# Optimization experiments

Hardware: AMD Instinct MI355X
Metric: run time of the kernel (lower is better)

## Reference

```python
import jax, jax.numpy as jnp
import numpy as np

N_USERS = 120000
N_ITEMS = 80000
N_NODES = N_USERS + N_ITEMS
D = 64
H = 2
DK = 32
DV = 32
N_LAYERS = 3
N_EDGES = 1280000
B = 4096
TEMPERATURE = 1.0


def setup_inputs() -> dict:
    key = jax.random.key(0)
    ks = jax.random.split(key, 11)
    glorot = lambda k, shape: jax.random.normal(k, shape, dtype=jnp.float32) * np.sqrt(2.0 / (shape[0] + int(np.prod(shape[1:]))))
    return {
        "edge_src": jax.random.randint(ks[0], (N_EDGES,), 0, N_NODES, dtype=jnp.int32),
        "edge_dst": jax.random.randint(ks[1], (N_EDGES,), 0, N_NODES, dtype=jnp.int32),
        # normalized adjacency values (positive, small) like D^-1/2 A D^-1/2 entries
        "edge_val": jax.random.uniform(ks[2], (N_EDGES,), dtype=jnp.float32) * 0.2,
        "U_emb": jax.random.normal(ks[3], (N_USERS, D), dtype=jnp.float32) * 0.01,
        "V_emb": jax.random.normal(ks[4], (N_ITEMS, D), dtype=jnp.float32) * 0.01,
        "Wq": glorot(ks[5], (D, H, DK)),
        "Wk": glorot(ks[6], (D, H, DK)),
        "Wv": glorot(ks[7], (D, H, DV)),
        "Wo": glorot(ks[8], (H * DV, D)),
        "u": jax.random.randint(ks[9], (B,), 0, N_USERS, dtype=jnp.int32),
        "i": jax.random.randint(ks[10], (B,), 0, N_ITEMS, dtype=jnp.int32),
    }


def reference(edge_src, edge_dst, edge_val, U_emb, V_emb, Wq, Wk, Wv, Wo, u, i):
    E0 = jnp.concatenate([U_emb, V_emb], axis=0)  # (N, d)

    # LightGCN propagation: E_{l+1} = A_norm @ E_l via edge-list scatter-add
    def prop(E, _):
        msg = edge_val[:, None] * E[edge_src]                      # (E, d) gather
        En = jax.ops.segment_sum(msg, edge_dst, num_segments=N_NODES)  # (N, d) scatter
        return En, En

    _, layer_outs = jax.lax.scan(prop, E0, None, length=N_LAYERS)
    Es = jnp.concatenate([E0[None], layer_outs], axis=0)  # (L, N, d), L = n_layers+1

    # Layer-wise QKV attention: Q from E0, K/V from every layer
    Q = jnp.einsum('nd,dhk->nhk', E0, Wq)        # (N, H, dk)
    K = jnp.einsum('lnd,dhk->lnhk', Es, Wk)      # (L, N, H, dk)
    V = jnp.einsum('lnd,dhv->lnhv', Es, Wv)      # (L, N, H, dv)
    scale = jnp.sqrt(jnp.asarray(DK, dtype=Q.dtype))
    scores = jnp.einsum('lnhk,nhk->lnh', K, Q) / scale
    alphas = jax.nn.softmax(scores / TEMPERATURE, axis=0)  # softmax over layers
    heads = jnp.einsum('lnh,lnhv->nhv', alphas, V)          # (N, H, dv)
    E_out = heads.reshape(N_NODES, H * DV) @ Wo             # (N, d)

    # score(u, i): dot product of final user/item embeddings
    Ue = E_out[u]
    Ie = E_out[N_USERS + i]
    return jnp.sum(Ue * Ie, axis=1)  # (B,)
```

## Files before the change

### kernel.cpp

```cpp
#include <hip/hip_runtime.h>
#include <hip/hip_fp16.h>

#define NU 120000
#define NI 80000
#define NN 200000
#define DD 64
#define NE 1280000
#define BB 4096
#define NS 8192
#define NB2 196
#define BCAP 8192
#define CH2 2048
#define CB 625

#define FB 196
#define CONVB 3125
#define PREPB 64
#define BSB 32
#define P1B 2048
#define G0B 512
#define NLB 32

__global__ void k_pre(int* __restrict__ bcur, int* __restrict__ n2cnt) {
  int t = threadIdx.x;
  if (t < NB2) bcur[t] = 0;
  if (t == 0) *n2cnt = 0;
}

__global__ void k_coarse2(const int* __restrict__ src, const int* __restrict__ dst,
                          const float* __restrict__ val, int* __restrict__ bcur,
                          int2* __restrict__ c_sv) {
  __shared__ int2 sv[CH2];
  __shared__ unsigned char map8[CH2];
  __shared__ int hist[256];
  __shared__ int lbase[256];
  __shared__ int gbase[256];
  __shared__ int s[256];
  int t = threadIdx.x;
  hist[t] = 0;
  __syncthreads();
  int e0 = blockIdx.x * CH2;
  int d_[CH2 / 256];
#pragma unroll
  for (int k = 0; k < CH2 / 256; ++k) {
    int e = e0 + k * 256 + t;
    d_[k] = (e < NE) ? dst[e] : -1;
    if (d_[k] >= 0) atomicAdd(&hist[d_[k] >> 10], 1);
  }
  __syncthreads();
  int x = hist[t];
  s[t] = x;
  __syncthreads();
  for (int off = 1; off < 256; off <<= 1) {
    int v = (t >= off) ? s[t - off] : 0;
    __syncthreads();
    s[t] += v;
    __syncthreads();
  }
  int lb = s[t] - x;
  lbase[t] = lb;
  gbase[t] = (x && t < NB2) ? (t * BCAP + atomicAdd(&bcur[t], x)) : 0;
  for (int k = lb; k < lb + x; ++k) map8[k] = (unsigned char)t;
  hist[t] = 0;
  __syncthreads();
#pragma unroll
  for (int k = 0; k < CH2 / 256; ++k) {
    int e = e0 + k * 256 + t;
    if (d_[k] >= 0) {
      int b = d_[k] >> 10;
      int lp = lbase[b] + atomicAdd(&hist[b], 1);
      sv[lp] = make_int2(src[e] | ((d_[k] & 1023) << 18), __float_as_int(val[e]));
    }
  }
  __syncthreads();
  int nval = NE - e0;
  if (nval > CH2) nval = CH2;
  for (int sidx = t; sidx < nval; sidx += 256) {
    int b = map8[sidx];
    c_sv[(size_t)gbase[b] + sidx - lbase[b]] = sv[sidx];
  }
}

__device__ __forceinline__ void d_conv(int rel, const float4* __restrict__ U4,
                                       const float4* __restrict__ V4, uint2* __restrict__ H0) {
  int t = threadIdx.x;
  float4 r[4];
#pragma unroll
  for (int k = 0; k < 4; ++k) {
    int idx = rel * 1024 + k * 256 + t;
    int node = idx >> 4, q = idx & 15;
    r[k] = (node < NU) ? U4[(size_t)node * 16 + q] : V4[(size_t)(node - NU) * 16 + q];
  }
#pragma unroll
  for (int k = 0; k < 4; ++k) {
    int idx = rel * 1024 + k * 256 + t;
    __half2 a = __floats2half2_rn(r[k].x, r[k].y);
    __half2 b = __floats2half2_rn(r[k].z, r[k].w);
    uint2 o;
    o.x = __builtin_bit_cast(unsigned int, a);
    o.y = __builtin_bit_cast(unsigned int, b);
    H0[idx] = o;
  }
}

__device__ __forceinline__ void d_prep(int rel, const float* __restrict__ Wq,
                                       const float* __restrict__ Wk, const float* __restrict__ Wv,
                                       const float* __restrict__ Wo, float* __restrict__ Mt,
                                       float* __restrict__ P) {
  int t = rel * 256 + threadIdx.x;
  if (t < 8192) {
    int h = t >> 12;
    int b = (t >> 6) & 63;
    int j = t & 63;
    float s = 0.f;
    for (int k = 0; k < 32; ++k) s += Wk[j * 64 + h * 32 + k] * Wq[b * 64 + h * 32 + k];
    Mt[h * 4096 + b * 64 + j] = s;
  } else if (t < 16384) {
    int t2 = t - 8192;
    int h = t2 >> 12;
    int d = (t2 >> 6) & 63;
    int j = t2 & 63;
    float s = 0.f;
    for (int v = 0; v < 32; ++v) s += Wv[d * 64 + h * 32 + v] * Wo[(h * 32 + v) * 64 + j];
    P[h * 4096 + d * 64 + j] = s;
  }
}

__global__ void k_fine4m(const int* __restrict__ bcur, const int2* __restrict__ c_sv,
                         int2* __restrict__ pairs, int* __restrict__ row_ptr,
                         const float4* __restrict__ U4, const float4* __restrict__ V4,
                         uint2* __restrict__ H0, const float* __restrict__ Wq,
                         const float* __restrict__ Wk, const float* __restrict__ Wv,
                         const float* __restrict__ Wo, float* __restrict__ Mt,
                         float* __restrict__ P, const int* __restrict__ u,
                         const int* __restrict__ ii, int* __restrict__ snodes) {
  __shared__ int cnt[1024];
  __shared__ int pre[1024];
  __shared__ int cur[1024];
  __shared__ int s[256];
  __shared__ int bs[256];
  int b = blockIdx.x, t = threadIdx.x;
  if (b >= FB) {
    int r = b - FB;
    if (r < CONVB) {
      d_conv(r, U4, V4, H0);
    } else if (r < CONVB + PREPB) {
      d_prep(r - CONVB, Wq, Wk, Wv, Wo, Mt, P);
    } else {
      int tt = (r - CONVB - PREPB) * 256 + t;
      if (tt < NS) snodes[tt] = (tt < BB) ? u[tt] : NU + ii[tt - BB];
    }
    return;
  }
  int bc = (t < NB2) ? bcur[t] : 0;
  bs[t] = bc;
  __syncthreads();
  for (int off = 1; off < 256; off <<= 1) {
    int v = (t >= off) ? bs[t - off] : 0;
    __syncthreads();
    bs[t] += v;
    __syncthreads();
  }
  int segN = bcur[b];
  int out0 = bs[b] - segN;
  int seg0 = b * BCAP;
  for (int k = t; k < 1024; k += 256) cnt[k] = 0;
  __syncthreads();
  for (int e = t; e < segN; e += 256) atomicAdd(&cnt[(c_sv[seg0 + e].x >> 18) & 1023], 1);
  __syncthreads();
  int a0 = cnt[4 * t], a1 = cnt[4 * t + 1], a2 = cnt[4 * t + 2], a3 = cnt[4 * t + 3];
  int tot = a0 + a1 + a2 + a3;
  s[t] = tot;
  __syncthreads();
  for (int off = 1; off < 256; off <<= 1) {
    int v = (t >= off) ? s[t - off] : 0;
    __syncthreads();
    s[t] += v;
    __syncthreads();
  }
  int base = s[t] - tot;
  pre[4 * t] = base;
  pre[4 * t + 1] = base + a0;
  pre[4 * t + 2] = base + a0 + a1;
  pre[4 * t + 3] = base + a0 + a1 + a2;
  int node0 = b << 10;
#pragma unroll
  for (int k = 0; k < 4; ++k) {
    int n = node0 + 4 * t + k;
    if (n < NN) row_ptr[n] = out0 + pre[4 * t + k];
  }
  if (b == 0 && t == 0) row_ptr[NN] = NE;
  for (int k = t; k < 1024; k += 256) cur[k] = 0;
  __syncthreads();
  for (int e = t; e < segN; e += 256) {
    int2 svv = c_sv[seg0 + e];
    int ld = (svv.x >> 18) & 1023;
    int off = atomicAdd(&cur[ld], 1);
    pairs[out0 + pre[ld] + off] = make_int2(svv.x & 0x3FFFF, svv.y);
  }
}

template <int ULIST, int BYPOS, int OUTF32>
__device__ __forceinline__ void d_prop8(const uint4* __restrict__ Hin4,
                                        uint4* __restrict__ Hout4, float4* __restrict__ Fout,
                                        const int* __restrict__ row_ptr,
                                        const int2* __restrict__ pairs,
                                        const int* __restrict__ list,
                                        const int* __restrict__ countp, int cconst, int relbid,
                                        int nblk) {
  int n = countp ? *countp : cconst;
  int lane = threadIdx.x & 63;
  int c = lane & 7;
  int gb = lane & 56;
  int gstride = (nblk * 256) >> 3;
  for (int gid = (relbid * 256 + (int)threadIdx.x) >> 3; gid < n; gid += gstride) {
    int node = ULIST ? list[gid] : gid;
    int start = row_ptr[node], end = row_ptr[node + 1];
    float4 a0 = make_float4(0.f, 0.f, 0.f, 0.f);
    float4 a1 = make_float4(0.f, 0.f, 0.f, 0.f);
    for (int t0 = start; t0 < end; t0 += 8) {
      int cap = end - t0;
      if (cap > 8) cap = 8;
      int2 mp = pairs[t0 + (c < cap ? c : 0)];
      uint4 r[8];
      float vv[8];
#pragma unroll
      for (int k = 0; k < 8; ++k) {
        int srclane = gb + k;
        int sidx = __shfl(mp.x, srclane);
        float v = __int_as_float(__shfl(mp.y, srclane));
        vv[k] = (k < cap) ? v : 0.f;
        r[k] = Hin4[(size_t)sidx * 8 + c];
      }
#pragma unroll
      for (int k = 0; k < 8; ++k) {
        float2 f0 = __half22float2(__builtin_bit_cast(__half2, r[k].x));
        float2 f1 = __half22float2(__builtin_bit_cast(__half2, r[k].y));
        float2 f2 = __half22float2(__builtin_bit_cast(__half2, r[k].z));
        float2 f3 = __half22float2(__builtin_bit_cast(__half2, r[k].w));
        a0.x += vv[k] * f0.x;
        a0.y += vv[k] * f0.y;
        a0.z += vv[k] * f1.x;
        a0.w += vv[k] * f1.y;
        a1.x += vv[k] * f2.x;
        a1.y += vv[k] * f2.y;
        a1.z += vv[k] * f3.x;
        a1.w += vv[k] * f3.y;
      }
    }
    size_t op = BYPOS ? (size_t)gid : (size_t)node;
    if (OUTF32) {
      Fout[op * 16 + 2 * c] = a0;
      Fout[op * 16 + 2 * c + 1] = a1;
    } else {
      uint4 o;
      o.x = __builtin_bit_cast(unsigned int, __floats2half2_rn(a0.x, a0.y));
      o.y = __builtin_bit_cast(unsigned int, __floats2half2_rn(a0.z, a0.w));
      o.z = __builtin_bit_cast(unsigned int, __floats2half2_rn(a1.x, a1.y));
      o.w = __builtin_bit_cast(unsigned int, __floats2half2_rn(a1.z, a1.w));
      Hout4[op * 8 + c] = o;
    }
  }
}

__device__ __forceinline__ void d_gather_h(int rel, const uint2* __restrict__ Htab,
                                           float4* __restrict__ Es_l,
                                           const int* __restrict__ snodes) {
  int t = rel * 256 + threadIdx.x;
  if (t >= NS * 16) return;
  int p = t >> 4, q = t & 15;
  int node = snodes[p];
  uint2 r = Htab[(size_t)node * 16 + q];
  float2 f0 = __half22float2(__builtin_bit_cast(__half2, r.x));
  float2 f1 = __half22float2(__builtin_bit_cast(__half2, r.y));
  Es_l[p * 16 + q] = make_float4(f0.x, f0.y, f1.x, f1.y);
}

__global__ void k_prop1m(const uint4* __restrict__ H04, uint4* __restrict__ H14,
                         const float4* __restrict__ U4, const float4* __restrict__ V4,
                         float4* __restrict__ Es0, const int* __restrict__ snodes,
                         const int* __restrict__ row_ptr, const int2* __restrict__ pairs,
                         int* __restrict__ n2list, int* __restrict__ n2cnt) {
  int b = blockIdx.x;
  if (b < P1B) {
    d_prop8<0, 0, 0>(H04, H14, nullptr, row_ptr, pairs, nullptr, nullptr, NN, b, P1B);
  } else if (b < P1B + G0B) {
    int t = (b - P1B) * 256 + threadIdx.x;
    if (t < NS * 16) {
      int p = t >> 4, q = t & 15;
      int node = snodes[p];
      Es0[p * 16 + q] =
          (node < NU) ? U4[(size_t)node * 16 + q] : V4[(size_t)(node - NU) * 16 + q];
    }
  } else {
    int idx = (b - P1B - G0B) * 256 + threadIdx.x;
    if (idx < NS) {
      int node = snodes[idx];
      int s0 = row_ptr[node], e0 = row_ptr[node + 1];
      int pos = atomicAdd(n2cnt, e0 - s0 + 1);
      n2list[pos++] = node;
      for (int j = s0; j < e0; ++j) n2list[pos++] = pairs[j].x;
    }
  }
}

__global__ void k_stage2(const uint4* __restrict__ H14, uint4* __restrict__ H24,
                         const uint2* __restrict__ H1, float4* __restrict__ Es1,
                         const int* __restrict__ snodes, const int* __restrict__ row_ptr,
                         const int2* __restrict__ pairs, const int* __restrict__ n2list,
                         const int* __restrict__ n2cnt) {
  int b = blockIdx.x;
  if (b < 512) {
    d_gather_h(b, H1, Es1, snodes);
  } else {
    d_prop8<1, 0, 0>(H14, H24, nullptr, row_ptr, pairs, n2list, n2cnt, 0, b - 512, 1024);
  }
}

__global__ void k_stage3(const uint4* __restrict__ H24, const uint2* __restrict__ H2,
                         float4* __restrict__ Es2, float4* __restrict__ Es3,
                         const int* __restrict__ snodes, const int* __restrict__ row_ptr,
                         const int2* __restrict__ pairs) {
  int b = blockIdx.x;
  if (b < 512) {
    d_gather_h(b, H2, Es2, snodes);
  } else {
    d_prop8<1, 1, 1>(H24, nullptr, Es3, row_ptr, pairs, snodes, nullptr, NS, b - 512, 512);
  }
}

__global__ void k_attn3(const float* __restrict__ Es, const float* __restrict__ Mt,
                        const float* __restrict__ P, float* __restrict__ out) {
  __shared__ float sb[4][3 * 64];
  int wv = threadIdx.x >> 6, lane = threadIdx.x & 63;
  int w = blockIdx.x * 4 + wv;
  if (w >= BB) return;
  const float inv_scale = 0.17677669529663687f;
  const float* M0 = Mt;
  const float* M1 = Mt + 4096;
  const float* P0 = P;
  const float* P1 = P + 4096;
  float eo[2];
#pragma unroll
  for (int side = 0; side < 2; ++side) {
    int p = side ? (BB + w) : w;
    float e0 = Es[(size_t)0 * NS * DD + p * DD + lane];
    float e1 = Es[(size_t)1 * NS * DD + p * DD + lane];
    float e2 = Es[(size_t)2 * NS * DD + p * DD + lane];
    float e3 = Es[(size_t)3 * NS * DD + p * DD + lane];
    sb[wv][lane] = e0;

    float g0 = 0.f, g1 = 0.f;
#pragma unroll 8
    for (int b = 0; b < 64; ++b) {
      float eb = sb[wv][b];
      g0 = fmaf(M0[b * 64 + lane], eb, g0);
      g1 = fmaf(M1[b * 64 + lane], eb, g1);
    }

    float el[4] = {e0, e1, e2, e3};
    float sc[4][2];
#pragma unroll
    for (int l = 0; l < 4; ++l) {
      float p0 = el[l] * g0, p1 = el[l] * g1;
#pragma unroll
      for (int o = 32; o; o >>= 1) {
        p0 += __shfl_xor(p0, o);
        p1 += __shfl_xor(p1, o);
      }
      sc[l][0] = p0 * inv_scale;
      sc[l][1] = p1 * inv_scale;
    }

    float ebar[2];
#pragma unroll
    for (int h = 0; h < 2; ++h) {
      float m = fmaxf(fmaxf(sc[0][h], sc[1][h]), fmaxf(sc[2][h], sc[3][h]));
      float x0 = expf(sc[0][h] - m), x1 = expf(sc[1][h] - m);
      float x2 = expf(sc[2][h] - m), x3 = expf(sc[3][h] - m);
      float inv = 1.f / (x0 + x1 + x2 + x3);
      ebar[h] = (x0 * e0 + x1 * e1 + x2 * e2 + x3 * e3) * inv;
    }
    sb[wv][64 + lane] = ebar[0];
    sb[wv][128 + lane] = ebar[1];

    float o = 0.f;
#pragma unroll 8
    for (int d = 0; d < 64; ++d) {
      float b0 = sb[wv][64 + d];
      float b1 = sb[wv][128 + d];
      o = fmaf(P0[d * 64 + lane], b0, o);
      o = fmaf(P1[d * 64 + lane], b1, o);
    }
    eo[side] = o;
  }
  float pd = eo[0] * eo[1];
#pragma unroll
  for (int o = 32; o; o >>= 1) pd += __shfl_xor(pd, o);
  if (lane == 0) out[w] = pd;
}

extern "C" void kernel_launch(void* const* d_in, const int* in_sizes, int n_in,
                              void* d_out, int out_size, void* d_ws, size_t ws_size,
                              hipStream_t stream) {
  const int* edge_src = (const int*)d_in[0];
  const int* edge_dst = (const int*)d_in[1];
  const float* edge_val = (const float*)d_in[2];
  const float* U_emb = (const float*)d_in[3];
  const float* V_emb = (const float*)d_in[4];
  const float* Wq = (const float*)d_in[5];
  const float* Wk = (const float*)d_in[6];
  const float* Wv = (const float*)d_in[7];
  const float* Wo = (const float*)d_in[8];
  const int* u = (const int*)d_in[9];
  const int* ii = (const int*)d_in[10];
  float* out = (float*)d_out;

  const float4* U4 = (const float4*)U_emb;
  const float4* V4 = (const float4*)V_emb;

  float* Ea = (float*)d_ws;
  float* Eb = Ea + (size_t)NN * DD;
  float* Es = Eb + (size_t)NN * DD;
  float* Mt = Es + (size_t)4 * NS * DD;
  float* Pm = Mt + 8192;
  int* row_ptr = (int*)(Pm + 8192);
  int* bcur = row_ptr + NN + 4;
  int* snodes = bcur + NB2;
  int* n2cnt = snodes + NS;
  uintptr_t pa = (uintptr_t)(n2cnt + 1);
  pa = (pa + 15) & ~(uintptr_t)15;
  int2* pairs = (int2*)pa;

  uint2* H0 = (uint2*)Ea;
  uint2* H1 = H0 + (size_t)NN * 16;
  uint2* H2 = (uint2*)Eb;
  int2* c_sv = (int2*)Eb;
  int* n2list = (int*)(Es + (size_t)3 * NS * DD);

  float4* Es4 = (float4*)Es;

  k_pre<<<1, 256, 0, stream>>>(bcur, n2cnt);
  k_coarse2<<<CB, 256, 0, stream>>>(edge_src, edge_dst, edge_val, bcur, c_sv);
  k_fine4m<<<FB + CONVB + PREPB + BSB, 256, 0, stream>>>(bcur, c_sv, pairs, row_ptr, U4, V4, H0,
                                                         Wq, Wk, Wv, Wo, Mt, Pm, u, ii, snodes);
  k_prop1m<<<P1B + G0B + NLB, 256, 0, stream>>>((const uint4*)H0, (uint4*)H1, U4, V4,
                                                Es4 + (size_t)0 * NS * 16, snodes, row_ptr, pairs,
                                                n2list, n2cnt);
  k_stage2<<<512 + 1024, 256, 0, stream>>>((const uint4*)H1, (uint4*)H2, H1,
                                           Es4 + (size_t)1 * NS * 16, snodes, row_ptr, pairs,
                                           n2list, n2cnt);
  k_stage3<<<512 + 512, 256, 0, stream>>>((const uint4*)H2, H2, Es4 + (size_t)2 * NS * 16,
                                          Es4 + (size_t)3 * NS * 16, snodes, row_ptr, pairs);
  k_attn3<<<(BB + 3) / 4, 256, 0, stream>>>(Es, Mt, Pm, out);
}
```

Before: 134.7 us.

## Merge pipeline stages into one persistent cooperative kernel with grid syncs

Replaces the seven kernel launches with one cooperative persistent kernel of 512 blocks that runs the phases with grid-stride loops separated by grid.sync(). It also rebalances the work: the coarse bucketing chunk size changes and the prep, zeroing and conversion work is merged into one phase. This removes launch gaps and the tail effects between stages. In exchange each phase gets fewer blocks, so the memory-bound propagation stages may have less parallelism, and every grid barrier has a cost. A fallback multi-kernel path runs if the cooperative launch fails.

```diff
diff --git a/kernel.cpp b/kernel.cpp
--- a/kernel.cpp
+++ b/kernel.cpp
@@ -1,5 +1,6 @@
 #include <hip/hip_runtime.h>
 #include <hip/hip_fp16.h>
+#include <hip/hip_cooperative_groups.h>
 
 #define NU 120000
 #define NI 80000
@@ -10,194 +11,209 @@
 #define NS 8192
 #define NB2 196
 #define BCAP 8192
-#define CH2 2048
-#define CB 625
-
-#define FB 196
-#define CONVB 3125
-#define PREPB 64
-#define BSB 32
-#define P1B 2048
-#define G0B 512
-#define NLB 32
-
-__global__ void k_pre(int* __restrict__ bcur, int* __restrict__ n2cnt) {
+#define CH2 1280
+#define NCH 1000
+#define GRID 512
+#define GSZ (GRID * 256)
+
+namespace cg = cooperative_groups;
+
+union SharedU {
+  struct {
+    int2 sv[CH2];
+    unsigned char map8[CH2];
+    int hist[256], lbase[256], gbase[256], s[256];
+  } co;
+  struct {
+    int cnt[1024], pre[1024], cur[1024];
+    int s[256], bs[256];
+  } fi;
+  struct {
+    float sb[4][192];
+  } at;
+};
+
+__device__ __forceinline__ void d_phaseA(int gtid, int stride, const float4* __restrict__ U4,
+                                         const float4* __restrict__ V4, uint2* __restrict__ H0,
+                                         const float* __restrict__ Wq,
+                                         const float* __restrict__ Wk,
+                                         const float* __restrict__ Wv,
+                                         const float* __restrict__ Wo, float* __restrict__ Mt,
+                                         float* __restrict__ Pm, const int* __restrict__ u,
+                                         const int* __restrict__ ii, int* __restrict__ snodes,
+                                         int* __restrict__ bcur, int* __restrict__ n2cnt) {
+  const int NCONV = NN * 16;
+  const int TOT = NCONV + 16384 + NS + 256;
+  for (int i = gtid; i < TOT; i += stride) {
+    if (i < NCONV) {
+      int node = i >> 4, q = i & 15;
+      float4 r = (node < NU) ? U4[(size_t)node * 16 + q] : V4[(size_t)(node - NU) * 16 + q];
+      uint2 o;
+      o.x = __builtin_bit_cast(unsigned int, __floats2half2_rn(r.x, r.y));
+      o.y = __builtin_bit_cast(unsigned int, __floats2half2_rn(r.z, r.w));
+      H0[(size_t)node * 16 + q] = o;
+    } else if (i < NCONV + 16384) {
+      int tt = i - NCONV;
+      if (tt < 8192) {
+        int h = tt >> 12, bb = (tt >> 6) & 63, j = tt & 63;
+        float sa = 0.f;
+        for (int k = 0; k < 32; ++k) sa += Wk[j * 64 + h * 32 + k] * Wq[bb * 64 + h * 32 + k];
+        Mt[h * 4096 + bb * 64 + j] = sa;
+      } else {
+        int t2 = tt - 8192;
+        int h = t2 >> 12, d = (t2 >> 6) & 63, j = t2 & 63;
+        float sa = 0.f;
+        for (int v = 0; v < 32; ++v) sa += Wv[d * 64 + h * 32 + v] * Wo[(h * 32 + v) * 64 + j];
+        Pm[h * 4096 + d * 64 + j] = sa;
+      }
+    } else if (i < NCONV + 16384 + NS) {
+      int tt = i - NCONV - 16384;
+      snodes[tt] = (tt < BB) ? u[tt] : NU + ii[tt - BB];
+    } else {
+      int z = i - NCONV - 16384 - NS;
+      if (z < NB2) bcur[z] = 0;
+      else if (z == NB2) *n2cnt = 0;
+    }
+  }
+}
+
+__device__ __forceinline__ void d_coarse_chunks(int b0, int nblk, const int* __restrict__ src,
+                                                const int* __restrict__ dst,
+                                                const float* __restrict__ val,
+                                                int* __restrict__ bcur, int2* __restrict__ c_sv,
+                                                SharedU& sh) {
   int t = threadIdx.x;
-  if (t < NB2) bcur[t] = 0;
-  if (t == 0) *n2cnt = 0;
-}
-
-__global__ void k_coarse2(const int* __restrict__ src, const int* __restrict__ dst,
-                          const float* __restrict__ val, int* __restrict__ bcur,
-                          int2* __restrict__ c_sv) {
-  __shared__ int2 sv[CH2];
-  __shared__ unsigned char map8[CH2];
-  __shared__ int hist[256];
-  __shared__ int lbase[256];
-  __shared__ int gbase[256];
-  __shared__ int s[256];
+  for (int ch = b0; ch < NCH; ch += nblk) {
+    sh.co.hist[t] = 0;
+    __syncthreads();
+    int e0 = ch * CH2;
+    int d_[CH2 / 256];
+#pragma unroll
+    for (int k = 0; k < CH2 / 256; ++k) {
+      int e = e0 + k * 256 + t;
+      d_[k] = dst[e];
+      atomicAdd(&sh.co.hist[d_[k] >> 10], 1);
+    }
+    __syncthreads();
+    int x = sh.co.hist[t];
+    sh.co.s[t] = x;
+    __syncthreads();
+    for (int off = 1; off < 256; off <<= 1) {
+      int v = (t >= off) ? sh.co.s[t - off] : 0;
+      __syncthreads();
+      sh.co.s[t] += v;
+      __syncthreads();
+    }
+    int lb = sh.co.s[t] - x;
+    sh.co.lbase[t] = lb;
+    sh.co.gbase[t] = (x && t < NB2) ? (t * BCAP + atomicAdd(&bcur[t], x)) : 0;
+    for (int k = lb; k < lb + x; ++k) sh.co.map8[k] = (unsigned char)t;
+    sh.co.hist[t] = 0;
+    __syncthreads();
+#pragma unroll
+    for (int k = 0; k < CH2 / 256; ++k) {
+      int e = e0 + k * 256 + t;
+      int bk = d_[k] >> 10;
+      int lp = sh.co.lbase[bk] + atomicAdd(&sh.co.hist[bk], 1);
+      sh.co.sv[lp] = make_int2(src[e] | ((d_[k] & 1023) << 18), __float_as_int(val[e]));
+    }
+    __syncthreads();
+    for (int sidx = t; sidx < CH2; sidx += 256) {
+      int bk = sh.co.map8[sidx];
+      c_sv[(size_t)sh.co.gbase[bk] + sidx - sh.co.lbase[bk]] = sh.co.sv[sidx];
+    }
+    __syncthreads();
+  }
+}
+
+__device__ __forceinline__ void d_fine_bucket(int b, const int* __restrict__ bcur,
+                                              const int2* __restrict__ c_sv,
+                                              int2* __restrict__ pairs,
+                                              int* __restrict__ row_ptr, SharedU& sh) {
   int t = threadIdx.x;
-  hist[t] = 0;
-  __syncthreads();
-  int e0 = blockIdx.x * CH2;
-  int d_[CH2 / 256];
-#pragma unroll
-  for (int k = 0; k < CH2 / 256; ++k) {
-    int e = e0 + k * 256 + t;
-    d_[k] = (e < NE) ? dst[e] : -1;
-    if (d_[k] >= 0) atomicAdd(&hist[d_[k] >> 10], 1);
-  }
-  __syncthreads();
-  int x = hist[t];
-  s[t] = x;
+  int bc = (t < NB2) ? bcur[t] : 0;
+  sh.fi.bs[t] = bc;
   __syncthreads();
   for (int off = 1; off < 256; off <<= 1) {
-    int v = (t >= off) ? s[t - off] : 0;
-    __syncthreads();
-    s[t] += v;
-    __syncthreads();
-  }
-  int lb = s[t] - x;
-  lbase[t] = lb;
-  gbase[t] = (x && t < NB2) ? (t * BCAP + atomicAdd(&bcur[t], x)) : 0;
-  for (int k = lb; k < lb + x; ++k) map8[k] = (unsigned char)t;
-  hist[t] = 0;
+    int v = (t >= off) ? sh.fi.bs[t - off] : 0;
+    __syncthreads();
+    sh.fi.bs[t] += v;
+    __syncthreads();
+  }
+  int segN = bcur[b];
+  int out0 = sh.fi.bs[b] - segN;
+  int seg0 = b * BCAP;
+  for (int k = t; k < 1024; k += 256) sh.fi.cnt[k] = 0;
   __syncthreads();
-#pragma unroll
-  for (int k = 0; k < CH2 / 256; ++k) {
-    int e = e0 + k * 256 + t;
-    if (d_[k] >= 0) {
-      int b = d_[k] >> 10;
-      int lp = lbase[b] + atomicAdd(&hist[b], 1);
-      sv[lp] = make_int2(src[e] | ((d_[k] & 1023) << 18), __float_as_int(val[e]));
-    }
-  }
+  for (int e = t; e < segN; e += 256) atomicAdd(&sh.fi.cnt[(c_sv[seg0 + e].x >> 18) & 1023], 1);
   __syncthreads();
-  int nval = NE - e0;
-  if (nval > CH2) nval = CH2;
-  for (int sidx = t; sidx < nval; sidx += 256) {
-    int b = map8[sidx];
-    c_sv[(size_t)gbase[b] + sidx - lbase[b]] = sv[sidx];
-  }
-}
-
-__device__ __forceinline__ void d_conv(int rel, const float4* __restrict__ U4,
-                                       const float4* __restrict__ V4, uint2* __restrict__ H0) {
-  int t = threadIdx.x;
-  float4 r[4];
-#pragma unroll
-  for (int k = 0; k < 4; ++k) {
-    int idx = rel * 1024 + k * 256 + t;
-    int node = idx >> 4, q = idx & 15;
-    r[k] = (node < NU) ? U4[(size_t)node * 16 + q] : V4[(size_t)(node - NU) * 16 + q];
-  }
-#pragma unroll
-  for (int k = 0; k < 4; ++k) {
-    int idx = rel * 1024 + k * 256 + t;
-    __half2 a = __floats2half2_rn(r[k].x, r[k].y);
-    __half2 b = __floats2half2_rn(r[k].z, r[k].w);
-    uint2 o;
-    o.x = __builtin_bit_cast(unsigned int, a);
-    o.y = __builtin_bit_cast(unsigned int, b);
-    H0[idx] = o;
-  }
-}
-
-__device__ __forceinline__ void d_prep(int rel, const float* __restrict__ Wq,
-                                       const float* __restrict__ Wk, const float* __restrict__ Wv,
-                                       const float* __restrict__ Wo, float* __restrict__ Mt,
-                                       float* __restrict__ P) {
-  int t = rel * 256 + threadIdx.x;
-  if (t < 8192) {
-    int h = t >> 12;
-    int b = (t >> 6) & 63;
-    int j = t & 63;
-    float s = 0.f;
-    for (int k = 0; k < 32; ++k) s += Wk[j * 64 + h * 32 + k] * Wq[b * 64 + h * 32 + k];
-    Mt[h * 4096 + b * 64 + j] = s;
-  } else if (t < 16384) {
-    int t2 = t - 8192;
-    int h = t2 >> 12;
-    int d = (t2 >> 6) & 63;
-    int j = t2 & 63;
-    float s = 0.f;
-    for (int v = 0; v < 32; ++v) s += Wv[d * 64 + h * 32 + v] * Wo[(h * 32 + v) * 64 + j];
-    P[h * 4096 + d * 64 + j] = s;
-  }
-}
-
-__global__ void k_fine4m(const int* __restrict__ bcur, const int2* __restrict__ c_sv,
-                         int2* __restrict__ pairs, int* __restrict__ row_ptr,
-                         const float4* __restrict__ U4, const float4* __restrict__ V4,
-                         uint2* __restrict__ H0, const float* __restrict__ Wq,
-                         const float* __restrict__ Wk, const float* __restrict__ Wv,
-                         const float* __restrict__ Wo, float* __restrict__ Mt,
-                         float* __restrict__ P, const int* __restrict__ u,
-                         const int* __restrict__ ii, int* __restrict__ snodes) {
-  __shared__ int cnt[1024];
-  __shared__ int pre[1024];
-  __shared__ int cur[1024];
-  __shared__ int s[256];
-  __shared__ int bs[256];
-  int b = blockIdx.x, t = threadIdx.x;
-  if (b >= FB) {
-    int r = b - FB;
-    if (r < CONVB) {
-      d_conv(r, U4, V4, H0);
-    } else if (r < CONVB + PREPB) {
-      d_prep(r - CONVB, Wq, Wk, Wv, Wo, Mt, P);
-    } else {
-      int tt = (r - CONVB - PREPB) * 256 + t;
-      if (tt < NS) snodes[tt] = (tt < BB) ? u[tt] : NU + ii[tt - BB];
-    }
-    return;
-  }
-  int bc = (t < NB2) ? bcur[t] : 0;
-  bs[t] = bc;
+  int a0 = sh.fi.cnt[4 * t], a1 = sh.fi.cnt[4 * t + 1];
+  int a2 = sh.fi.cnt[4 * t + 2], a3 = sh.fi.cnt[4 * t + 3];
+  int tot = a0 + a1 + a2 + a3;
+  sh.fi.s[t] = tot;
   __syncthreads();
   for (int off = 1; off < 256; off <<= 1) {
-    int v = (t >= off) ? bs[t - off] : 0;
-    __syncthreads();
-    bs[t] += v;
-    __syncthreads();
-  }
-  int segN = bcur[b];
-  int out0 = bs[b] - segN;
-  int seg0 = b * BCAP;
-  for (int k = t; k < 1024; k += 256) cnt[k] = 0;
-  __syncthreads();
-  for (int e = t; e < segN; e += 256) atomicAdd(&cnt[(c_sv[seg0 + e].x >> 18) & 1023], 1);
-  __syncthreads();
-  int a0 = cnt[4 * t], a1 = cnt[4 * t + 1], a2 = cnt[4 * t + 2], a3 = cnt[4 * t + 3];
-  int tot = a0 + a1 + a2 + a3;
-  s[t] = tot;
-  __syncthreads();
-  for (int off = 1; off < 256; off <<= 1) {
-    int v = (t >= off) ? s[t - off] : 0;
-    __syncthreads();
-    s[t] += v;
-    __syncthreads();
-  }
-  int base = s[t] - tot;
-  pre[4 * t] = base;
-  pre[4 * t + 1] = base + a0;
-  pre[4 * t + 2] = base + a0 + a1;
-  pre[4 * t + 3] = base + a0 + a1 + a2;
+    int v = (t >= off) ? sh.fi.s[t - off] : 0;
+    __syncthreads();
+    sh.fi.s[t] += v;
+    __syncthreads();
+  }
+  int base = sh.fi.s[t] - tot;
+  sh.fi.pre[4 * t] = base;
+  sh.fi.pre[4 * t + 1] = base + a0;
+  sh.fi.pre[4 * t + 2] = base + a0 + a1;
+  sh.fi.pre[4 * t + 3] = base + a0 + a1 + a2;
   int node0 = b << 10;
 #pragma unroll
   for (int k = 0; k < 4; ++k) {
     int n = node0 + 4 * t + k;
-    if (n < NN) row_ptr[n] = out0 + pre[4 * t + k];
+    if (n < NN) row_ptr[n] = out0 + sh.fi.pre[4 * t + k];
   }
   if (b == 0 && t == 0) row_ptr[NN] = NE;
-  for (int k = t; k < 1024; k += 256) cur[k] = 0;
+  for (int k = t; k < 1024; k += 256) sh.fi.cur[k] = 0;
   __syncthreads();
   for (int e = t; e < segN; e += 256) {
     int2 svv = c_sv[seg0 + e];
     int ld = (svv.x >> 18) & 1023;
-    int off = atomicAdd(&cur[ld], 1);
-    pairs[out0 + pre[ld] + off] = make_int2(svv.x & 0x3FFFF, svv.y);
-  }
+    int off = atomicAdd(&sh.fi.cur[ld], 1);
+    pairs[out0 + sh.fi.pre[ld] + off] = make_int2(svv.x & 0x3FFFF, svv.y);
+  }
+}
+
+__device__ __forceinline__ void d_gather0_gs(int rel, int nblk, const float4* __restrict__ U4,
+                                             const float4* __restrict__ V4,
+                                             float4* __restrict__ Es0,
+                                             const int* __restrict__ snodes) {
+  for (int i = rel * 256 + (int)threadIdx.x; i < NS * 16; i += nblk * 256) {
+    int p = i >> 4, q = i & 15;
+    int node = snodes[p];
+    Es0[p * 16 + q] = (node < NU) ? U4[(size_t)node * 16 + q] : V4[(size_t)(node - NU) * 16 + q];
+  }
+}
+
+__device__ __forceinline__ void d_gather_h_gs(int rel, int nblk, const uint2* __restrict__ Htab,
+                                              float4* __restrict__ Es_l,
+                                              const int* __restrict__ snodes) {
+  for (int i = rel * 256 + (int)threadIdx.x; i < NS * 16; i += nblk * 256) {
+    int p = i >> 4, q = i & 15;
+    int node = snodes[p];
+    uint2 r = Htab[(size_t)node * 16 + q];
+    float2 f0 = __half22float2(__builtin_bit_cast(__half2, r.x));
+    float2 f1 = __half22float2(__builtin_bit_cast(__half2, r.y));
+    Es_l[p * 16 + q] = make_float4(f0.x, f0.y, f1.x, f1.y);
+  }
+}
+
+__device__ __forceinline__ void d_nbr(int idx, const int* __restrict__ snodes,
+                                      const int* __restrict__ row_ptr,
+                                      const int2* __restrict__ pairs, int* __restrict__ n2list,
+                                      int* __restrict__ n2cnt) {
+  if (idx >= NS) return;
+  int node = snodes[idx];
+  int s0 = row_ptr[node], e0 = row_ptr[node + 1];
+  int pos = atomicAdd(n2cnt, e0 - s0 + 1);
+  n2list[pos++] = node;
+  for (int j = s0; j < e0; ++j) n2list[pos++] = pairs[j].x;
 }
 
 template <int ULIST, int BYPOS, int OUTF32>
@@ -263,141 +279,160 @@
   }
 }
 
-__device__ __forceinline__ void d_gather_h(int rel, const uint2* __restrict__ Htab,
-                                           float4* __restrict__ Es_l,
-                                           const int* __restrict__ snodes) {
-  int t = rel * 256 + threadIdx.x;
-  if (t >= NS * 16) return;
-  int p = t >> 4, q = t & 15;
-  int node = snodes[p];
-  uint2 r = Htab[(size_t)node * 16 + q];
-  float2 f0 = __half22float2(__builtin_bit_cast(__half2, r.x));
-  float2 f1 = __half22float2(__builtin_bit_cast(__half2, r.y));
-  Es_l[p * 16 + q] = make_float4(f0.x, f0.y, f1.x, f1.y);
-}
-
-__global__ void k_prop1m(const uint4* __restrict__ H04, uint4* __restrict__ H14,
-                         const float4* __restrict__ U4, const float4* __restrict__ V4,
-                         float4* __restrict__ Es0, const int* __restrict__ snodes,
-                         const int* __restrict__ row_ptr, const int2* __restrict__ pairs,
-                         int* __restrict__ n2list, int* __restrict__ n2cnt) {
-  int b = blockIdx.x;
-  if (b < P1B) {
-    d_prop8<0, 0, 0>(H04, H14, nullptr, row_ptr, pairs, nullptr, nullptr, NN, b, P1B);
-  } else if (b < P1B + G0B) {
-    int t = (b - P1B) * 256 + threadIdx.x;
-    if (t < NS * 16) {
-      int p = t >> 4, q = t & 15;
-      int node = snodes[p];
-      Es0[p * 16 + q] =
-          (node < NU) ? U4[(size_t)node * 16 + q] : V4[(size_t)(node - NU) * 16 + q];
-    }
-  } else {
-    int idx = (b - P1B - G0B) * 256 + threadIdx.x;
-    if (idx < NS) {
-      int node = snodes[idx];
-      int s0 = row_ptr[node], e0 = row_ptr[node + 1];
-      int pos = atomicAdd(n2cnt, e0 - s0 + 1);
-      n2list[pos++] = node;
-      for (int j = s0; j < e0; ++j) n2list[pos++] = pairs[j].x;
-    }
-  }
-}
-
-__global__ void k_stage2(const uint4* __restrict__ H14, uint4* __restrict__ H24,
-                         const uint2* __restrict__ H1, float4* __restrict__ Es1,
-                         const int* __restrict__ snodes, const int* __restrict__ row_ptr,
-                         const int2* __restrict__ pairs, const int* __restrict__ n2list,
-                         const int* __restrict__ n2cnt) {
-  int b = blockIdx.x;
-  if (b < 512) {
-    d_gather_h(b, H1, Es1, snodes);
-  } else {
-    d_prop8<1, 0, 0>(H14, H24, nullptr, row_ptr, pairs, n2list, n2cnt, 0, b - 512, 1024);
-  }
-}
-
-__global__ void k_stage3(const uint4* __restrict__ H24, const uint2* __restrict__ H2,
-                         float4* __restrict__ Es2, float4* __restrict__ Es3,
-                         const int* __restrict__ snodes, const int* __restrict__ row_ptr,
-                         const int2* __restrict__ pairs) {
-  int b = blockIdx.x;
-  if (b < 512) {
-    d_gather_h(b, H2, Es2, snodes);
-  } else {
-    d_prop8<1, 1, 1>(H24, nullptr, Es3, row_ptr, pairs, snodes, nullptr, NS, b - 512, 512);
-  }
-}
-
-__global__ void k_attn3(const float* __restrict__ Es, const float* __restrict__ Mt,
-                        const float* __restrict__ P, float* __restrict__ out) {
-  __shared__ float sb[4][3 * 64];
+__device__ __forceinline__ void d_attn_gs(int b, int nblk, const float* __restrict__ Es,
+                                          const float* __restrict__ Mt,
+                                          const float* __restrict__ Pm, float* __restrict__ out,
+                                          float* sbw) {
   int wv = threadIdx.x >> 6, lane = threadIdx.x & 63;
-  int w = blockIdx.x * 4 + wv;
-  if (w >= BB) return;
+  (void)wv;
   const float inv_scale = 0.17677669529663687f;
   const float* M0 = Mt;
   const float* M1 = Mt + 4096;
-  const float* P0 = P;
-  const float* P1 = P + 4096;
-  float eo[2];
-#pragma unroll
-  for (int side = 0; side < 2; ++side) {
-    int p = side ? (BB + w) : w;
-    float e0 = Es[(size_t)0 * NS * DD + p * DD + lane];
-    float e1 = Es[(size_t)1 * NS * DD + p * DD + lane];
-    float e2 = Es[(size_t)2 * NS * DD + p * DD + lane];
-    float e3 = Es[(size_t)3 * NS * DD + p * DD + lane];
-    sb[wv][lane] = e0;
-
-    float g0 = 0.f, g1 = 0.f;
+  const float* P0 = Pm;
+  const float* P1 = Pm + 4096;
+  for (int wi = b; wi * 4 < BB; wi += nblk) {
+    int w = wi * 4 + (threadIdx.x >> 6);
+    float eo[2];
+#pragma unroll
+    for (int side = 0; side < 2; ++side) {
+      int p = side ? (BB + w) : w;
+      float e0 = Es[(size_t)0 * NS * DD + p * DD + lane];
+      float e1 = Es[(size_t)1 * NS * DD + p * DD + lane];
+      float e2 = Es[(size_t)2 * NS * DD + p * DD + lane];
+      float e3 = Es[(size_t)3 * NS * DD + p * DD + lane];
+      sbw[lane] = e0;
+
+      float g0 = 0.f, g1 = 0.f;
 #pragma unroll 8
-    for (int b = 0; b < 64; ++b) {
-      float eb = sb[wv][b];
-      g0 = fmaf(M0[b * 64 + lane], eb, g0);
-      g1 = fmaf(M1[b * 64 + lane], eb, g1);
-    }
-
-    float el[4] = {e0, e1, e2, e3};
-    float sc[4][2];
-#pragma unroll
-    for (int l = 0; l < 4; ++l) {
-      float p0 = el[l] * g0, p1 = el[l] * g1;
-#pragma unroll
-      for (int o = 32; o; o >>= 1) {
-        p0 += __shfl_xor(p0, o);
-        p1 += __shfl_xor(p1, o);
-      }
-      sc[l][0] = p0 * inv_scale;
-      sc[l][1] = p1 * inv_scale;
-    }
-
-    float ebar[2];
-#pragma unroll
-    for (int h = 0; h < 2; ++h) {
-      float m = fmaxf(fmaxf(sc[0][h], sc[1][h]), fmaxf(sc[2][h], sc[3][h]));
-      float x0 = expf(sc[0][h] - m), x1 = expf(sc[1][h] - m);
-      float x2 = expf(sc[2][h] - m), x3 = expf(sc[3][h] - m);
-      float inv = 1.f / (x0 + x1 + x2 + x3);
-      ebar[h] = (x0 * e0 + x1 * e1 + x2 * e2 + x3 * e3) * inv;
-    }
-    sb[wv][64 + lane] = ebar[0];
-    sb[wv][128 + lane] = ebar[1];
-
-    float o = 0.f;
+      for (int bb = 0; bb < 64; ++bb) {
+        float eb = sbw[bb];
+        g0 = fmaf(M0[bb * 64 + lane], eb, g0);
+        g1 = fmaf(M1[bb * 64 + lane], eb, g1);
+      }
+
+      float el[4] = {e0, e1, e2, e3};
+      float sc[4][2];
+#pragma unroll
+      for (int l = 0; l < 4; ++l) {
+        float p0 = el[l] * g0, p1 = el[l] * g1;
+#pragma unroll
+        for (int o = 32; o; o >>= 1) {
+          p0 += __shfl_xor(p0, o);
+          p1 += __shfl_xor(p1, o);
+        }
+        sc[l][0] = p0 * inv_scale;
+        sc[l][1] = p1 * inv_scale;
+      }
+
+      float ebar[2];
+#pragma unroll
+      for (int h = 0; h < 2; ++h) {
+        float m = fmaxf(fmaxf(sc[0][h], sc[1][h]), fmaxf(sc[2][h], sc[3][h]));
+        float x0 = expf(sc[0][h] - m), x1 = expf(sc[1][h] - m);
+        float x2 = expf(sc[2][h] - m), x3 = expf(sc[3][h] - m);
+        float inv = 1.f / (x0 + x1 + x2 + x3);
+        ebar[h] = (x0 * e0 + x1 * e1 + x2 * e2 + x3 * e3) * inv;
+      }
+      sbw[64 + lane] = ebar[0];
+      sbw[128 + lane] = ebar[1];
+
+      float o = 0.f;
 #pragma unroll 8
-    for (int d = 0; d < 64; ++d) {
-      float b0 = sb[wv][64 + d];
-      float b1 = sb[wv][128 + d];
-      o = fmaf(P0[d * 64 + lane], b0, o);
-      o = fmaf(P1[d * 64 + lane], b1, o);
-    }
-    eo[side] = o;
-  }
-  float pd = eo[0] * eo[1];
-#pragma unroll
-  for (int o = 32; o; o >>= 1) pd += __shfl_xor(pd, o);
-  if (lane == 0) out[w] = pd;
+      for (int d = 0; d < 64; ++d) {
+        float b0 = sbw[64 + d];
+        float b1 = sbw[128 + d];
+        o = fmaf(P0[d * 64 + lane], b0, o);
+        o = fmaf(P1[d * 64 + lane], b1, o);
+      }
+      eo[side] = o;
+    }
+    float pd = eo[0] * eo[1];
+#pragma unroll
+    for (int o = 32; o; o >>= 1) pd += __shfl_xor(pd, o);
+    if (lane == 0) out[w] = pd;
+  }
+}
+
+__global__ void __launch_bounds__(256, 2)
+k_mega(const int* __restrict__ src, const int* __restrict__ dst, const float* __restrict__ val,
+       const float4* __restrict__ U4, const float4* __restrict__ V4,
+       const float* __restrict__ Wq, const float* __restrict__ Wk,
+       const float* __restrict__ Wv, const float* __restrict__ Wo, const int* __restrict__ u,
+       const int* __restrict__ ii, uint2* __restrict__ H0, uint2* __restrict__ H1,
+       uint2* __restrict__ H2, float4* __restrict__ Es4, float* __restrict__ Mt,
+       float* __restrict__ Pm, int* __restrict__ row_ptr, int* __restrict__ bcur,
+       int* __restrict__ snodes, int* __restrict__ n2cnt, int2* __restrict__ pairs,
+       int2* __restrict__ c_sv, int* __restrict__ n2list, float* __restrict__ out) {
+  __shared__ SharedU sh;
+  cg::grid_group grid = cg::this_grid();
+  int b = blockIdx.x, t = threadIdx.x;
+
+  d_phaseA(b * 256 + t, GSZ, U4, V4, H0, Wq, Wk, Wv, Wo, Mt, Pm, u, ii, snodes, bcur, n2cnt);
+  grid.sync();
+
+  d_coarse_chunks(b, GRID, src, dst, val, bcur, c_sv, sh);
+  grid.sync();
+
+  if (b < NB2) d_fine_bucket(b, bcur, c_sv, pairs, row_ptr, sh);
+  else d_gather0_gs(b - NB2, GRID - NB2, U4, V4, Es4, snodes);
+  grid.sync();
+
+  if (b < 32) d_nbr(b * 256 + t, snodes, row_ptr, pairs, n2list, n2cnt);
+  else d_prop8<0, 0, 0>((const uint4*)H0, (uint4*)H1, nullptr, row_ptr, pairs, nullptr, nullptr,
+                        NN, b - 32, GRID - 32);
+  grid.sync();
+
+  if (b < 128) d_gather_h_gs(b, 128, H1, Es4 + (size_t)1 * NS * 16, snodes);
+  else d_prop8<1, 0, 0>((const uint4*)H1, (uint4*)H2, nullptr, row_ptr, pairs, n2list, n2cnt, 0,
+                        b - 128, GRID - 128);
+  grid.sync();
+
+  if (b < 128) d_gather_h_gs(b, 128, H2, Es4 + (size_t)2 * NS * 16, snodes);
+  else d_prop8<1, 1, 1>((const uint4*)H2, nullptr, Es4 + (size_t)3 * NS * 16, row_ptr, pairs,
+                        snodes, nullptr, NS, b - 128, GRID - 128);
+  grid.sync();
+
+  d_attn_gs(b, GRID, (const float*)Es4, Mt, Pm, out, sh.at.sb[t >> 6]);
+}
+
+__global__ void fb_A(const float4* U4, const float4* V4, uint2* H0, const float* Wq,
+                     const float* Wk, const float* Wv, const float* Wo, float* Mt, float* Pm,
+                     const int* u, const int* ii, int* snodes, int* bcur, int* n2cnt) {
+  d_phaseA(blockIdx.x * 256 + threadIdx.x, 1024 * 256, U4, V4, H0, Wq, Wk, Wv, Wo, Mt, Pm, u, ii,
+           snodes, bcur, n2cnt);
+}
+__global__ void fb_B(const int* src, const int* dst, const float* val, int* bcur, int2* c_sv) {
+  __shared__ SharedU sh;
+  d_coarse_chunks(blockIdx.x, NCH, src, dst, val, bcur, c_sv, sh);
+}
+__global__ void fb_C(const int* bcur, const int2* c_sv, int2* pairs, int* row_ptr,
+                     const float4* U4, const float4* V4, float4* Es0, const int* snodes) {
+  __shared__ SharedU sh;
+  if (blockIdx.x < NB2) d_fine_bucket(blockIdx.x, bcur, c_sv, pairs, row_ptr, sh);
+  else d_gather0_gs(blockIdx.x - NB2, 512, U4, V4, Es0, snodes);
+}
+__global__ void fb_D(const uint4* H04, uint4* H14, const int* row_ptr, const int2* pairs,
+                     const int* snodes, int* n2list, int* n2cnt) {
+  if (blockIdx.x < 32) d_nbr(blockIdx.x * 256 + threadIdx.x, snodes, row_ptr, pairs, n2list, n2cnt);
+  else d_prop8<0, 0, 0>(H04, H14, nullptr, row_ptr, pairs, nullptr, nullptr, NN, blockIdx.x - 32,
+                        2048);
+}
+__global__ void fb_E(const uint4* H14, uint4* H24, const uint2* H1, float4* Es1,
+                     const int* snodes, const int* row_ptr, const int2* pairs, const int* n2list,
+                     const int* n2cnt) {
+  if (blockIdx.x < 512) d_gather_h_gs(blockIdx.x, 512, H1, Es1, snodes);
+  else d_prop8<1, 0, 0>(H14, H24, nullptr, row_ptr, pairs, n2list, n2cnt, 0, blockIdx.x - 512,
+                        1024);
+}
+__global__ void fb_F(const uint4* H24, const uint2* H2, float4* Es2, float4* Es3,
+                     const int* snodes, const int* row_ptr, const int2* pairs) {
+  if (blockIdx.x < 512) d_gather_h_gs(blockIdx.x, 512, H2, Es2, snodes);
+  else d_prop8<1, 1, 1>(H24, nullptr, Es3, row_ptr, pairs, snodes, nullptr, NS, blockIdx.x - 512,
+                        512);
+}
+__global__ void fb_G(const float* Es, const float* Mt, const float* Pm, float* out) {
+  __shared__ SharedU sh;
+  d_attn_gs(blockIdx.x, 1024, Es, Mt, Pm, out, sh.at.sb[threadIdx.x >> 6]);
 }
 
 extern "C" void kernel_launch(void* const* d_in, const int* in_sizes, int n_in,
@@ -406,8 +441,8 @@
   const int* edge_src = (const int*)d_in[0];
   const int* edge_dst = (const int*)d_in[1];
   const float* edge_val = (const float*)d_in[2];
-  const float* U_emb = (const float*)d_in[3];
-  const float* V_emb = (const float*)d_in[4];
+  const float4* U4 = (const float4*)d_in[3];
+  const float4* V4 = (const float4*)d_in[4];
   const float* Wq = (const float*)d_in[5];
   const float* Wk = (const float*)d_in[6];
   const float* Wv = (const float*)d_in[7];
@@ -415,9 +450,6 @@
   const int* u = (const int*)d_in[9];
   const int* ii = (const int*)d_in[10];
   float* out = (float*)d_out;
-
-  const float4* U4 = (const float4*)U_emb;
-  const float4* V4 = (const float4*)V_emb;
 
   float* Ea = (float*)d_ws;
   float* Eb = Ea + (size_t)NN * DD;
@@ -440,17 +472,27 @@
 
   float4* Es4 = (float4*)Es;
 
-  k_pre<<<1, 256, 0, stream>>>(bcur, n2cnt);
-  k_coarse2<<<CB, 256, 0, stream>>>(edge_src, edge_dst, edge_val, bcur, c_sv);
-  k_fine4m<<<FB + CONVB + PREPB + BSB, 256, 0, stream>>>(bcur, c_sv, pairs, row_ptr, U4, V4, H0,
-                                                         Wq, Wk, Wv, Wo, Mt, Pm, u, ii, snodes);
-  k_prop1m<<<P1B + G0B + NLB, 256, 0, stream>>>((const uint4*)H0, (uint4*)H1, U4, V4,
-                                                Es4 + (size_t)0 * NS * 16, snodes, row_ptr, pairs,
-                                                n2list, n2cnt);
-  k_stage2<<<512 + 1024, 256, 0, stream>>>((const uint4*)H1, (uint4*)H2, H1,
-                                           Es4 + (size_t)1 * NS * 16, snodes, row_ptr, pairs,
-                                           n2list, n2cnt);
-  k_stage3<<<512 + 512, 256, 0, stream>>>((const uint4*)H2, H2, Es4 + (size_t)2 * NS * 16,
-                                          Es4 + (size_t)3 * NS * 16, snodes, row_ptr, pairs);
-  k_attn3<<<(BB + 3) / 4, 256, 0, stream>>>(Es, Mt, Pm, out);
-}
+  void* args[] = {(void*)&edge_src, (void*)&edge_dst, (void*)&edge_val, (void*)&U4, (void*)&V4,
+                  (void*)&Wq,       (void*)&Wk,       (void*)&Wv,       (void*)&Wo, (void*)&u,
+                  (void*)&ii,       (void*)&H0,       (void*)&H1,       (void*)&H2, (void*)&Es4,
+                  (void*)&Mt,       (void*)&Pm,       (void*)&row_ptr,  (void*)&bcur,
+                  (void*)&snodes,   (void*)&n2cnt,    (void*)&pairs,    (void*)&c_sv,
+                  (void*)&n2list,   (void*)&out};
+  hipError_t err =
+      hipLaunchCooperativeKernel((const void*)k_mega, dim3(GRID), dim3(256), args, 0, stream);
+  if (err != hipSuccess) {
+    (void)hipGetLastError();
+    fb_A<<<1024, 256, 0, stream>>>(U4, V4, H0, Wq, Wk, Wv, Wo, Mt, Pm, u, ii, snodes, bcur,
+                                   n2cnt);
+    fb_B<<<NCH, 256, 0, stream>>>(edge_src, edge_dst, edge_val, bcur, c_sv);
+    fb_C<<<NB2 + 512, 256, 0, stream>>>(bcur, c_sv, pairs, row_ptr, U4, V4, Es4, snodes);
+    fb_D<<<32 + 2048, 256, 0, stream>>>((const uint4*)H0, (uint4*)H1, row_ptr, pairs, snodes,
+                                        n2list, n2cnt);
+    fb_E<<<512 + 1024, 256, 0, stream>>>((const uint4*)H1, (uint4*)H2, H1,
+                                         Es4 + (size_t)1 * NS * 16, snodes, row_ptr, pairs,
+                                         n2list, n2cnt);
+    fb_F<<<512 + 512, 256, 0, stream>>>((const uint4*)H2, H2, Es4 + (size_t)2 * NS * 16,
+                                        Es4 + (size_t)3 * NS * 16, snodes, row_ptr, pairs);
+    fb_G<<<1024, 256, 0, stream>>>((const float*)Es4, Mt, Pm, out);
+  }
+}
```

Measured after the change: 509.4 us. +278.1%, slower.
